# Performance work log

Measured on AMD Instinct MI355X. Metric: run time of the kernel, lower is better.

The kernel has to match this reference:

```python
import jax, jax.numpy as jnp
import numpy as np

N_NODES = 100000   # vertices
N_EDGES = 20000    # hyperedges
NNZ = 1600000      # incidence entries (avg vertex degree 16)
D_IN = 128
D_OUT = 128


def setup_inputs() -> dict:
    key = jax.random.key(0)
    k1, k2, k3, k4, k5 = jax.random.split(key, 5)
    X = jax.random.normal(k1, (N_NODES, D_IN), dtype=jnp.float32)
    v_idx = jax.random.randint(k2, (NNZ,), 0, N_NODES)
    e_idx = jax.random.randint(k3, (NNZ,), 0, N_EDGES)
    theta_w = jax.random.normal(k4, (D_IN, D_OUT), dtype=jnp.float32) / np.sqrt(D_IN)
    theta_b = jax.random.normal(k5, (D_OUT,), dtype=jnp.float32) * 0.01
    return {"X": X, "theta_w": theta_w, "theta_b": theta_b,
            "v_idx": v_idx, "e_idx": e_idx}


def reference(X, theta_w, theta_b, v_idx, e_idx):
    # degrees (edge weights w_e = 1)
    ones = jnp.ones(v_idx.shape[0], dtype=X.dtype)
    d_v = jax.ops.segment_sum(ones, v_idx, num_segments=N_NODES)   # [N]
    d_e = jax.ops.segment_sum(ones, e_idx, num_segments=N_EDGES)   # [M]
    inv_sqrt_dv = jnp.where(d_v > 0, d_v ** -0.5, 0.0)
    inv_de = jnp.where(d_e > 0, 1.0 / d_e, 0.0)

    # theta: dense GEMM
    Xt = X @ theta_w + theta_b                                     # [N, D_OUT]

    # smoothing_with_HGNN: D_v^{-1/2} H W D_e^{-1} H^T D_v^{-1/2} Xt
    Xs = Xt * inv_sqrt_dv[:, None]                                 # [N, D_OUT]
    Ye = jax.ops.segment_sum(Xs[v_idx], e_idx, num_segments=N_EDGES)  # H^T Xs -> [M, D_OUT]
    Ye = Ye * inv_de[:, None]
    Xv = jax.ops.segment_sum(Ye[e_idx], v_idx, num_segments=N_NODES)  # H Ye -> [N, D_OUT]
    return jax.nn.relu(Xv * inv_sqrt_dv[:, None])
```

## Files before the change

kernel.cpp:

```cpp
#include <hip/hip_runtime.h>

#define N_NODES 100000
#define N_EDGES 20000
#define NNZ     1600000
#define D       128
#define DW      64

#define NB      256
#define CAP_E   8192
#define CAP_V   8192
#define SPAN_E  ((N_EDGES + NB - 1) / NB)
#define SPAN_V  ((N_NODES + NB - 1) / NB)
#define P1_CHUNK 8192
#define P1_ITER  (P1_CHUNK / 256)
#define P1_BLOCKS ((NNZ + P1_CHUNK - 1) / P1_CHUNK)

typedef __attribute__((ext_vector_type(8))) short bf16x8;
typedef __attribute__((ext_vector_type(4))) float f32x4;

__device__ __forceinline__ unsigned int pack_bf2(float lo, float hi) {
  unsigned int ul = __float_as_uint(lo), uh = __float_as_uint(hi);
  ul = (ul + 0x7FFFu + ((ul >> 16) & 1u)) >> 16;
  uh = (uh + 0x7FFFu + ((uh >> 16) & 1u)) & 0xFFFF0000u;
  return ul | uh;
}

__global__ __launch_bounds__(256) void k_prep(const float* __restrict__ W, unsigned int* __restrict__ Wtp,
                                              int* __restrict__ ce, int* __restrict__ cv) {
  int t = threadIdx.x;
  if (blockIdx.x == 0) { ce[t] = t * CAP_E; cv[t] = t * CAP_V; }
  int idx = blockIdx.x * 256 + t;
  if (idx < D * DW) {
    int c = idx & 127, kp = idx >> 7;
    float lo = W[(size_t)(2 * kp) * D + c];
    float hi = W[(size_t)(2 * kp + 1) * D + c];
    Wtp[c * DW + kp] = pack_bf2(lo, hi);
  }
}

__global__ __launch_bounds__(256) void k_bin(const int* __restrict__ v_idx, const int* __restrict__ e_idx,
                                             int* __restrict__ ce, int* __restrict__ cv,
                                             unsigned int* __restrict__ Te, unsigned int* __restrict__ Tv) {
  __shared__ int he[NB], hv[NB], be[NB], bv[NB], le[NB], lv[NB];
  int t = threadIdx.x;
  he[t] = 0; hv[t] = 0; le[t] = 0; lv[t] = 0;
  __syncthreads();
  int base = blockIdx.x * P1_CHUNK;
  int v[P1_ITER], e[P1_ITER];
#pragma unroll
  for (int j = 0; j < P1_ITER; ++j) {
    int idx = base + j * 256 + t;
    if (idx < NNZ) {
      v[j] = v_idx[idx]; e[j] = e_idx[idx];
      atomicAdd(&he[e[j] / SPAN_E], 1);
      atomicAdd(&hv[v[j] / SPAN_V], 1);
    } else v[j] = -1;
  }
  __syncthreads();
  be[t] = he[t] ? atomicAdd(&ce[t], he[t]) : 0;
  bv[t] = hv[t] ? atomicAdd(&cv[t], hv[t]) : 0;
  __syncthreads();
#pragma unroll
  for (int j = 0; j < P1_ITER; ++j) {
    if (v[j] < 0) continue;
    int eb = e[j] / SPAN_E, vb = v[j] / SPAN_V;
    int se = be[eb] + atomicAdd(&le[eb], 1);
    int sv = bv[vb] + atomicAdd(&lv[vb], 1);
    if (se < (eb + 1) * CAP_E) Te[se] = ((unsigned)e[j] << 17) | (unsigned)v[j];
    if (sv < (vb + 1) * CAP_V) Tv[sv] = ((unsigned)v[j] << 15) | (unsigned)e[j];
  }
}

__global__ __launch_bounds__(256) void k_sort(const int* __restrict__ ce, const int* __restrict__ cv,
                                              unsigned int* __restrict__ Te, unsigned int* __restrict__ Tv,
                                              int* __restrict__ cnt_e, float* __restrict__ invde,
                                              int* __restrict__ starts_e,
                                              int* __restrict__ cnt_v, float* __restrict__ risv,
                                              int* __restrict__ starts_v,
                                              const float* __restrict__ X, unsigned int* __restrict__ Xs) {
  __shared__ unsigned int raw[CAP_V];
  __shared__ int hist[SPAN_V], lcur[SPAN_V], loff[SPAN_V + 1];
  __shared__ float rv[SPAN_V];
  int t = threadIdx.x;
  if (blockIdx.x < NB) {
    int b = blockIdx.x;
    int v0 = b * SPAN_V;
    int span = N_NODES - v0; if (span > SPAN_V) span = SPAN_V;
    if (span <= 0) return;
    int n = cv[b] - b * CAP_V; if (n > CAP_V) n = CAP_V; if (n < 0) n = 0;
    for (int i = t; i < n; i += 256) raw[i] = Tv[b * CAP_V + i];
    for (int i = t; i < span; i += 256) { hist[i] = 0; lcur[i] = 0; }
    __syncthreads();
    for (int i = t; i < n; i += 256) atomicAdd(&hist[(int)(raw[i] >> 15) - v0], 1);
    __syncthreads();
    if (t == 0) { int run = 0; for (int i = 0; i < span; ++i) { loff[i] = run; run += hist[i]; } loff[span] = run; }
    __syncthreads();
    for (int i = t; i < n; i += 256) {
      unsigned int p = raw[i];
      int l = (int)(p >> 15) - v0;
      int slot = loff[l] + atomicAdd(&lcur[l], 1);
      Tv[b * CAP_V + slot] = p & 0x7FFFu;
    }
    for (int i = t; i < span; i += 256) {
      int d = hist[i];
      float r = d > 0 ? rsqrtf((float)d) : 0.0f;
      cnt_v[v0 + i] = d;
      risv[v0 + i] = r;
      rv[i] = r;
      starts_v[v0 + i] = b * CAP_V + loff[i];
    }
    __syncthreads();
    int total = span * DW;
    for (int idx = t; idx < total; idx += 256) {
      int vl = idx >> 6;
      float r = rv[vl];
      size_t gp = (size_t)(v0 + vl) * DW + (idx & 63);
      float2 x = *(const float2*)(X + gp * 2);
      Xs[gp] = pack_bf2(r * x.x, r * x.y);
    }
  } else {
    int b = blockIdx.x - NB;
    int e0 = b * SPAN_E;
    int span = N_EDGES - e0; if (span > SPAN_E) span = SPAN_E;
    if (span <= 0) return;
    int n = ce[b] - b * CAP_E; if (n > CAP_E) n = CAP_E; if (n < 0) n = 0;
    for (int i = t; i < n; i += 256) raw[i] = Te[b * CAP_E + i];
    for (int i = t; i < span; i += 256) { hist[i] = 0; lcur[i] = 0; }
    __syncthreads();
    for (int i = t; i < n; i += 256) atomicAdd(&hist[(int)(raw[i] >> 17) - e0], 1);
    __syncthreads();
    if (t == 0) { int run = 0; for (int i = 0; i < span; ++i) { loff[i] = run; run += hist[i]; } loff[span] = run; }
    __syncthreads();
    for (int i = t; i < n; i += 256) {
      unsigned int p = raw[i];
      int l = (int)(p >> 17) - e0;
      int slot = loff[l] + atomicAdd(&lcur[l], 1);
      Te[b * CAP_E + slot] = p & 0x1FFFFu;
    }
    for (int i = t; i < span; i += 256) {
      int d = hist[i];
      cnt_e[e0 + i] = d;
      invde[e0 + i] = d > 0 ? 1.0f / (float)d : 0.0f;
      starts_e[e0 + i] = b * CAP_E + loff[i];
    }
  }
}

__global__ void k_edge_gather(const unsigned int* __restrict__ Xs, const float* __restrict__ risv,
                              const int* __restrict__ starts_e, const int* __restrict__ cnt_e,
                              const unsigned int* __restrict__ members,
                              unsigned int* __restrict__ Qeb, float* __restrict__ qv) {
  int wid = (blockIdx.x * 256 + threadIdx.x) >> 6;
  int lane = threadIdx.x & 63;
  if (wid >= N_EDGES) return;
  int beg = __builtin_amdgcn_readfirstlane(starts_e[wid]);
  int end = beg + __builtin_amdgcn_readfirstlane(cnt_e[wid]);
  float ax = 0.f, ay = 0.f, q = 0.f;
  int i = beg;
  for (; i + 16 <= end; i += 16) {
    int vv[16]; unsigned int xx[16];
#pragma unroll
    for (int j = 0; j < 16; ++j) vv[j] = members[i + j];
#pragma unroll
    for (int j = 0; j < 16; ++j) xx[j] = Xs[(size_t)vv[j] * DW + lane];
#pragma unroll
    for (int j = 0; j < 16; ++j) q += risv[vv[j]];
#pragma unroll
    for (int j = 0; j < 16; ++j) {
      ax += __uint_as_float(xx[j] << 16);
      ay += __uint_as_float(xx[j] & 0xFFFF0000u);
    }
  }
  if (i + 8 <= end) {
    int vv[8]; unsigned int xx[8];
#pragma unroll
    for (int j = 0; j < 8; ++j) vv[j] = members[i + j];
#pragma unroll
    for (int j = 0; j < 8; ++j) xx[j] = Xs[(size_t)vv[j] * DW + lane];
#pragma unroll
    for (int j = 0; j < 8; ++j) q += risv[vv[j]];
#pragma unroll
    for (int j = 0; j < 8; ++j) {
      ax += __uint_as_float(xx[j] << 16);
      ay += __uint_as_float(xx[j] & 0xFFFF0000u);
    }
    i += 8;
  }
  for (; i < end; ++i) {
    int v = members[i];
    unsigned int x = Xs[(size_t)v * DW + lane];
    ax += __uint_as_float(x << 16);
    ay += __uint_as_float(x & 0xFFFF0000u);
    q += risv[v];
  }
  Qeb[(size_t)wid * DW + lane] = pack_bf2(ax, ay);
  if (lane == 0) qv[wid] = q;
}

__global__ __launch_bounds__(256) void k_gemm(const unsigned int* __restrict__ Qeb, const float* __restrict__ qv,
                                              const unsigned int* __restrict__ Wtp, const float* __restrict__ bias,
                                              const float* __restrict__ invde, unsigned short* __restrict__ Yeb) {
  int wid = (blockIdx.x * 256 + threadIdx.x) >> 6;
  int lane = threadIdx.x & 63;
  if (wid >= N_EDGES / 16) return;
  int e0 = wid * 16;
  int lrow = lane & 15, lhalf = lane >> 4;
  const unsigned int* arow = Qeb + (size_t)(e0 + lrow) * DW + lhalf * 4;
  f32x4 acc[8];
#pragma unroll
  for (int nt = 0; nt < 8; ++nt) acc[nt] = (f32x4){0.f, 0.f, 0.f, 0.f};
#pragma unroll
  for (int kt = 0; kt < 4; ++kt) {
    bf16x8 a = *(const bf16x8*)(arow + kt * 16);
#pragma unroll
    for (int nt = 0; nt < 8; ++nt) {
      bf16x8 b = *(const bf16x8*)(Wtp + (size_t)(nt * 16 + lrow) * DW + kt * 16 + lhalf * 4);
      acc[nt] = __builtin_amdgcn_mfma_f32_16x16x32_bf16(a, b, acc[nt], 0, 0, 0);
    }
  }
#pragma unroll
  for (int r = 0; r < 4; ++r) {
    int row = e0 + lhalf * 4 + r;
    float s = invde[row], q = qv[row];
#pragma unroll
    for (int nt = 0; nt < 8; ++nt) {
      int c = nt * 16 + lrow;
      float val = s * (acc[nt][r] + q * bias[c]);
      unsigned int u = __float_as_uint(val);
      u = (u + 0x7FFFu + ((u >> 16) & 1u)) >> 16;
      Yeb[(size_t)row * D + c] = (unsigned short)u;
    }
  }
}

__global__ void k_vertex_gather(const unsigned int* __restrict__ Yeb, const float* __restrict__ risv,
                                const int* __restrict__ starts_v, const int* __restrict__ cnt_v,
                                const unsigned int* __restrict__ members,
                                float* __restrict__ out) {
  int wid = (blockIdx.x * 256 + threadIdx.x) >> 6;
  int lane = threadIdx.x & 63;
  if (wid >= N_NODES) return;
  int beg = __builtin_amdgcn_readfirstlane(starts_v[wid]);
  int end = beg + __builtin_amdgcn_readfirstlane(cnt_v[wid]);
  float ax = 0.f, ay = 0.f;
  int i = beg;
  for (; i + 16 <= end; i += 16) {
    int ee[16]; unsigned int yy[16];
#pragma unroll
    for (int j = 0; j < 16; ++j) ee[j] = members[i + j];
#pragma unroll
    for (int j = 0; j < 16; ++j) yy[j] = Yeb[(size_t)ee[j] * DW + lane];
#pragma unroll
    for (int j = 0; j < 16; ++j) {
      ax += __uint_as_float(yy[j] << 16);
      ay += __uint_as_float(yy[j] & 0xFFFF0000u);
    }
  }
  if (i + 8 <= end) {
    int ee[8]; unsigned int yy[8];
#pragma unroll
    for (int j = 0; j < 8; ++j) ee[j] = members[i + j];
#pragma unroll
    for (int j = 0; j < 8; ++j) yy[j] = Yeb[(size_t)ee[j] * DW + lane];
#pragma unroll
    for (int j = 0; j < 8; ++j) {
      ax += __uint_as_float(yy[j] << 16);
      ay += __uint_as_float(yy[j] & 0xFFFF0000u);
    }
    i += 8;
  }
  for (; i < end; ++i) {
    unsigned int y = Yeb[(size_t)members[i] * DW + lane];
    ax += __uint_as_float(y << 16);
    ay += __uint_as_float(y & 0xFFFF0000u);
  }
  float s = risv[wid];
  float2 o; o.x = fmaxf(ax * s, 0.f); o.y = fmaxf(ay * s, 0.f);
  *(float2*)(out + (size_t)wid * D + lane * 2) = o;
}

extern "C" void kernel_launch(void* const* d_in, const int* in_sizes, int n_in,
                              void* d_out, int out_size, void* d_ws, size_t ws_size,
                              hipStream_t stream) {
  const float* X    = (const float*)d_in[0];
  const float* W    = (const float*)d_in[1];
  const float* bias = (const float*)d_in[2];
  const int* v_idx  = (const int*)d_in[3];
  const int* e_idx  = (const int*)d_in[4];
  float* out = (float*)d_out;

  char* p = (char*)d_ws;
  auto alloc = [&](size_t bytes) { char* r = p; p += (bytes + 255) & ~(size_t)255; return r; };
  unsigned int* Te  = (unsigned int*)alloc((size_t)NB * CAP_E * 4);
  unsigned int* Tv  = (unsigned int*)alloc((size_t)NB * CAP_V * 4);
  unsigned int* Xs  = (unsigned int*)alloc((size_t)N_NODES * DW * 4);
  unsigned int* Qeb = (unsigned int*)alloc((size_t)N_EDGES * DW * 4);
  unsigned int* Yeb = (unsigned int*)alloc((size_t)N_EDGES * DW * 4);
  unsigned int* Wtp = (unsigned int*)alloc((size_t)D * DW * 4);
  float* qv    = (float*)alloc((size_t)N_EDGES * 4);
  float* risv  = (float*)alloc((size_t)N_NODES * 4);
  float* invde = (float*)alloc((size_t)N_EDGES * 4);
  int* cnt_e    = (int*)alloc((size_t)N_EDGES * 4);
  int* cnt_v    = (int*)alloc((size_t)N_NODES * 4);
  int* starts_e = (int*)alloc((size_t)N_EDGES * 4);
  int* starts_v = (int*)alloc((size_t)N_NODES * 4);
  int* ce       = (int*)alloc(NB * 4);
  int* cv       = (int*)alloc(NB * 4);

  k_prep<<<(D * DW + 255) / 256, 256, 0, stream>>>(W, Wtp, ce, cv);
  k_bin<<<P1_BLOCKS, 256, 0, stream>>>(v_idx, e_idx, ce, cv, Te, Tv);
  k_sort<<<2 * NB, 256, 0, stream>>>(ce, cv, Te, Tv, cnt_e, invde, starts_e,
                                     cnt_v, risv, starts_v, X, Xs);
  k_edge_gather<<<N_EDGES / 4, 256, 0, stream>>>(Xs, risv, starts_e, cnt_e, Te, Qeb, qv);
  k_gemm<<<(N_EDGES / 16 + 3) / 4, 256, 0, stream>>>(Qeb, qv, Wtp, bias, invde, (unsigned short*)Yeb);
  k_vertex_gather<<<N_NODES / 4, 256, 0, stream>>>(Yeb, risv, starts_v, cnt_v, Tv, out);
}
```

Baseline: 289.5 us.

## Split each wavefront into four 16-lane groups with uint4 row gathers

Both gather kernels now give each 16-lane quarter of a wavefront its own edge or vertex, so one wave handles four segments. Each lane loads a uint4 (8 bf16 values) per row instead of one packed pair. Padded sentinel rows (a zero row in Xs and Yeb, and a zero risv entry) let groups with shorter lists keep looping to the wave-wide maximum count without branching. This aims to cut per-segment wave overhead and issue fewer, wider memory requests. The cost is lanes doing wasted sentinel loads when degrees differ within a wave, plus reads of members past each segment's end.

```diff
diff --git a/kernel.cpp b/kernel.cpp
--- a/kernel.cpp
+++ b/kernel.cpp
@@ -26,9 +26,15 @@
 }
 
 __global__ __launch_bounds__(256) void k_prep(const float* __restrict__ W, unsigned int* __restrict__ Wtp,
-                                              int* __restrict__ ce, int* __restrict__ cv) {
+                                              int* __restrict__ ce, int* __restrict__ cv,
+                                              unsigned int* __restrict__ Xs, unsigned int* __restrict__ Yeb,
+                                              float* __restrict__ risv) {
   int t = threadIdx.x;
-  if (blockIdx.x == 0) { ce[t] = t * CAP_E; cv[t] = t * CAP_V; }
+  if (blockIdx.x == 0) {
+    ce[t] = t * CAP_E; cv[t] = t * CAP_V;
+    if (t < DW) { Xs[(size_t)N_NODES * DW + t] = 0u; Yeb[(size_t)N_EDGES * DW + t] = 0u; }
+    if (t == 0) risv[N_NODES] = 0.f;
+  }
   int idx = blockIdx.x * 256 + t;
   if (idx < D * DW) {
     int c = idx & 127, kp = idx >> 7;
@@ -146,55 +152,47 @@
   }
 }
 
-__global__ void k_edge_gather(const unsigned int* __restrict__ Xs, const float* __restrict__ risv,
+__global__ __launch_bounds__(256) void k_edge_gather(const unsigned int* __restrict__ Xs, const float* __restrict__ risv,
                               const int* __restrict__ starts_e, const int* __restrict__ cnt_e,
                               const unsigned int* __restrict__ members,
                               unsigned int* __restrict__ Qeb, float* __restrict__ qv) {
-  int wid = (blockIdx.x * 256 + threadIdx.x) >> 6;
+  int wv = (blockIdx.x * 256 + threadIdx.x) >> 6;
   int lane = threadIdx.x & 63;
-  if (wid >= N_EDGES) return;
-  int beg = __builtin_amdgcn_readfirstlane(starts_e[wid]);
-  int end = beg + __builtin_amdgcn_readfirstlane(cnt_e[wid]);
-  float ax = 0.f, ay = 0.f, q = 0.f;
-  int i = beg;
-  for (; i + 16 <= end; i += 16) {
-    int vv[16]; unsigned int xx[16];
-#pragma unroll
-    for (int j = 0; j < 16; ++j) vv[j] = members[i + j];
-#pragma unroll
-    for (int j = 0; j < 16; ++j) xx[j] = Xs[(size_t)vv[j] * DW + lane];
-#pragma unroll
-    for (int j = 0; j < 16; ++j) q += risv[vv[j]];
-#pragma unroll
-    for (int j = 0; j < 16; ++j) {
-      ax += __uint_as_float(xx[j] << 16);
-      ay += __uint_as_float(xx[j] & 0xFFFF0000u);
-    }
-  }
-  if (i + 8 <= end) {
-    int vv[8]; unsigned int xx[8];
-#pragma unroll
-    for (int j = 0; j < 8; ++j) vv[j] = members[i + j];
-#pragma unroll
-    for (int j = 0; j < 8; ++j) xx[j] = Xs[(size_t)vv[j] * DW + lane];
+  int g = lane >> 4, l16 = lane & 15;
+  int e = wv * 4 + g;
+  if (e >= N_EDGES) return;
+  int beg = starts_e[e];
+  int cnt = cnt_e[e];
+  int maxc = cnt;
+  maxc = max(maxc, __shfl_xor(maxc, 16));
+  maxc = max(maxc, __shfl_xor(maxc, 32));
+  float a0=0,a1=0,a2=0,a3=0,a4=0,a5=0,a6=0,a7=0,q=0.f;
+  for (int i = 0; i < maxc; i += 8) {
+    int vv[8];
+#pragma unroll
+    for (int j = 0; j < 8; ++j) {
+      int idx = i + j;
+      int m = (int)members[beg + idx];
+      vv[j] = (idx < cnt) ? m : N_NODES;
+    }
+    uint4 xx[8];
+#pragma unroll
+    for (int j = 0; j < 8; ++j) xx[j] = *(const uint4*)(Xs + (size_t)vv[j] * DW + l16 * 4);
 #pragma unroll
     for (int j = 0; j < 8; ++j) q += risv[vv[j]];
 #pragma unroll
     for (int j = 0; j < 8; ++j) {
-      ax += __uint_as_float(xx[j] << 16);
-      ay += __uint_as_float(xx[j] & 0xFFFF0000u);
-    }
-    i += 8;
-  }
-  for (; i < end; ++i) {
-    int v = members[i];
-    unsigned int x = Xs[(size_t)v * DW + lane];
-    ax += __uint_as_float(x << 16);
-    ay += __uint_as_float(x & 0xFFFF0000u);
-    q += risv[v];
-  }
-  Qeb[(size_t)wid * DW + lane] = pack_bf2(ax, ay);
-  if (lane == 0) qv[wid] = q;
+      a0 += __uint_as_float(xx[j].x << 16); a1 += __uint_as_float(xx[j].x & 0xFFFF0000u);
+      a2 += __uint_as_float(xx[j].y << 16); a3 += __uint_as_float(xx[j].y & 0xFFFF0000u);
+      a4 += __uint_as_float(xx[j].z << 16); a5 += __uint_as_float(xx[j].z & 0xFFFF0000u);
+      a6 += __uint_as_float(xx[j].w << 16); a7 += __uint_as_float(xx[j].w & 0xFFFF0000u);
+    }
+  }
+  uint4 o;
+  o.x = pack_bf2(a0, a1); o.y = pack_bf2(a2, a3);
+  o.z = pack_bf2(a4, a5); o.w = pack_bf2(a6, a7);
+  *(uint4*)(Qeb + (size_t)e * DW + l16 * 4) = o;
+  if (l16 == 0) qv[e] = q;
 }
 
 __global__ __launch_bounds__(256) void k_gemm(const unsigned int* __restrict__ Qeb, const float* __restrict__ qv,
@@ -233,50 +231,49 @@
   }
 }
 
-__global__ void k_vertex_gather(const unsigned int* __restrict__ Yeb, const float* __restrict__ risv,
+__global__ __launch_bounds__(256) void k_vertex_gather(const unsigned int* __restrict__ Yeb, const float* __restrict__ risv,
                                 const int* __restrict__ starts_v, const int* __restrict__ cnt_v,
                                 const unsigned int* __restrict__ members,
                                 float* __restrict__ out) {
-  int wid = (blockIdx.x * 256 + threadIdx.x) >> 6;
+  int wv = (blockIdx.x * 256 + threadIdx.x) >> 6;
   int lane = threadIdx.x & 63;
-  if (wid >= N_NODES) return;
-  int beg = __builtin_amdgcn_readfirstlane(starts_v[wid]);
-  int end = beg + __builtin_amdgcn_readfirstlane(cnt_v[wid]);
-  float ax = 0.f, ay = 0.f;
-  int i = beg;
-  for (; i + 16 <= end; i += 16) {
-    int ee[16]; unsigned int yy[16];
-#pragma unroll
-    for (int j = 0; j < 16; ++j) ee[j] = members[i + j];
-#pragma unroll
-    for (int j = 0; j < 16; ++j) yy[j] = Yeb[(size_t)ee[j] * DW + lane];
-#pragma unroll
-    for (int j = 0; j < 16; ++j) {
-      ax += __uint_as_float(yy[j] << 16);
-      ay += __uint_as_float(yy[j] & 0xFFFF0000u);
-    }
-  }
-  if (i + 8 <= end) {
-    int ee[8]; unsigned int yy[8];
-#pragma unroll
-    for (int j = 0; j < 8; ++j) ee[j] = members[i + j];
-#pragma unroll
-    for (int j = 0; j < 8; ++j) yy[j] = Yeb[(size_t)ee[j] * DW + lane];
+  int g = lane >> 4, l16 = lane & 15;
+  int v = wv * 4 + g;
+  if (v >= N_NODES) return;
+  int beg = starts_v[v];
+  int cnt = cnt_v[v];
+  int maxc = cnt;
+  maxc = max(maxc, __shfl_xor(maxc, 16));
+  maxc = max(maxc, __shfl_xor(maxc, 32));
+  float a0=0,a1=0,a2=0,a3=0,a4=0,a5=0,a6=0,a7=0;
+  for (int i = 0; i < maxc; i += 8) {
+    int ee[8];
 #pragma unroll
     for (int j = 0; j < 8; ++j) {
-      ax += __uint_as_float(yy[j] << 16);
-      ay += __uint_as_float(yy[j] & 0xFFFF0000u);
-    }
-    i += 8;
-  }
-  for (; i < end; ++i) {
-    unsigned int y = Yeb[(size_t)members[i] * DW + lane];
-    ax += __uint_as_float(y << 16);
-    ay += __uint_as_float(y & 0xFFFF0000u);
-  }
-  float s = risv[wid];
-  float2 o; o.x = fmaxf(ax * s, 0.f); o.y = fmaxf(ay * s, 0.f);
-  *(float2*)(out + (size_t)wid * D + lane * 2) = o;
+      int idx = i + j;
+      int m = (int)members[beg + idx];
+      ee[j] = (idx < cnt) ? m : N_EDGES;
+    }
+    uint4 yy[8];
+#pragma unroll
+    for (int j = 0; j < 8; ++j) yy[j] = *(const uint4*)(Yeb + (size_t)ee[j] * DW + l16 * 4);
+#pragma unroll
+    for (int j = 0; j < 8; ++j) {
+      a0 += __uint_as_float(yy[j].x << 16); a1 += __uint_as_float(yy[j].x & 0xFFFF0000u);
+      a2 += __uint_as_float(yy[j].y << 16); a3 += __uint_as_float(yy[j].y & 0xFFFF0000u);
+      a4 += __uint_as_float(yy[j].z << 16); a5 += __uint_as_float(yy[j].z & 0xFFFF0000u);
+      a6 += __uint_as_float(yy[j].w << 16); a7 += __uint_as_float(yy[j].w & 0xFFFF0000u);
+    }
+  }
+  float s = risv[v];
+  float4 o0, o1;
+  o0.x = fmaxf(a0 * s, 0.f); o0.y = fmaxf(a1 * s, 0.f);
+  o0.z = fmaxf(a2 * s, 0.f); o0.w = fmaxf(a3 * s, 0.f);
+  o1.x = fmaxf(a4 * s, 0.f); o1.y = fmaxf(a5 * s, 0.f);
+  o1.z = fmaxf(a6 * s, 0.f); o1.w = fmaxf(a7 * s, 0.f);
+  float* orow = out + (size_t)v * D + l16 * 8;
+  *(float4*)orow = o0;
+  *(float4*)(orow + 4) = o1;
 }
 
 extern "C" void kernel_launch(void* const* d_in, const int* in_sizes, int n_in,
@@ -293,12 +290,12 @@
   auto alloc = [&](size_t bytes) { char* r = p; p += (bytes + 255) & ~(size_t)255; return r; };
   unsigned int* Te  = (unsigned int*)alloc((size_t)NB * CAP_E * 4);
   unsigned int* Tv  = (unsigned int*)alloc((size_t)NB * CAP_V * 4);
-  unsigned int* Xs  = (unsigned int*)alloc((size_t)N_NODES * DW * 4);
+  unsigned int* Xs  = (unsigned int*)alloc((size_t)(N_NODES + 1) * DW * 4);
   unsigned int* Qeb = (unsigned int*)alloc((size_t)N_EDGES * DW * 4);
-  unsigned int* Yeb = (unsigned int*)alloc((size_t)N_EDGES * DW * 4);
+  unsigned int* Yeb = (unsigned int*)alloc((size_t)(N_EDGES + 1) * DW * 4);
   unsigned int* Wtp = (unsigned int*)alloc((size_t)D * DW * 4);
   float* qv    = (float*)alloc((size_t)N_EDGES * 4);
-  float* risv  = (float*)alloc((size_t)N_NODES * 4);
+  float* risv  = (float*)alloc((size_t)(N_NODES + 1) * 4);
   float* invde = (float*)alloc((size_t)N_EDGES * 4);
   int* cnt_e    = (int*)alloc((size_t)N_EDGES * 4);
   int* cnt_v    = (int*)alloc((size_t)N_NODES * 4);
@@ -307,11 +304,11 @@
   int* ce       = (int*)alloc(NB * 4);
   int* cv       = (int*)alloc(NB * 4);
 
-  k_prep<<<(D * DW + 255) / 256, 256, 0, stream>>>(W, Wtp, ce, cv);
+  k_prep<<<(D * DW + 255) / 256, 256, 0, stream>>>(W, Wtp, ce, cv, Xs, Yeb, risv);
   k_bin<<<P1_BLOCKS, 256, 0, stream>>>(v_idx, e_idx, ce, cv, Te, Tv);
   k_sort<<<2 * NB, 256, 0, stream>>>(ce, cv, Te, Tv, cnt_e, invde, starts_e,
                                      cnt_v, risv, starts_v, X, Xs);
-  k_edge_gather<<<N_EDGES / 4, 256, 0, stream>>>(Xs, risv, starts_e, cnt_e, Te, Qeb, qv);
+  k_edge_gather<<<(N_EDGES / 4 + 3) / 4, 256, 0, stream>>>(Xs, risv, starts_e, cnt_e, Te, Qeb, qv);
   k_gemm<<<(N_EDGES / 16 + 3) / 4, 256, 0, stream>>>(Qeb, qv, Wtp, bias, invde, (unsigned short*)Yeb);
-  k_vertex_gather<<<N_NODES / 4, 256, 0, stream>>>(Yeb, risv, starts_v, cnt_v, Tv, out);
-}
+  k_vertex_gather<<<(N_NODES / 4 + 3) / 4, 256, 0, stream>>>(Yeb, risv, starts_v, cnt_v, Tv, out);
+}
```

New measurement: 278.6 us. 3.7% less time.
